# Kernel tuning notes

Measured on AMD Instinct MI355X. Metric: run time of the kernel, lower is better.

Reference implementation:

```python
import jax, jax.numpy as jnp
import numpy as np

N_NODES = 50000
N_EDGES = 800000
NFEAT = 128
NHID = 64
NLAYER = 3
BN_EPS = 1e-5


def _bn(h, gamma, beta):
    # BatchNorm1d, training-mode batch statistics (biased variance)
    mu = jnp.mean(h, axis=0)
    var = jnp.mean((h - mu) ** 2, axis=0)
    return gamma * (h - mu) * jax.lax.rsqrt(var + BN_EPS) + beta


def setup_inputs() -> dict:
    key = jax.random.key(0)
    ks = jax.random.split(key, 8)
    x = jax.random.normal(ks[0], (N_NODES, NFEAT), dtype=jnp.float32)
    edge_index = jax.random.randint(ks[1], (2, N_EDGES), 0, N_NODES, dtype=jnp.int64)
    # transform: Linear(nfeat, nhid) with bias, then BN
    W_t = jax.random.normal(ks[2], (NFEAT, NHID), dtype=jnp.float32) / np.sqrt(NFEAT)
    b_t = jnp.zeros((NHID,), dtype=jnp.float32)
    g_t = jnp.ones((NHID,), dtype=jnp.float32)
    bb_t = jnp.zeros((NHID,), dtype=jnp.float32)
    # per-layer GIN MLPs (bias=False) and BN affine params, stacked over layers
    W1 = jax.random.normal(ks[3], (NLAYER, NHID, NHID), dtype=jnp.float32) / np.sqrt(NHID)
    W2 = jax.random.normal(ks[4], (NLAYER, NHID, NHID), dtype=jnp.float32) / np.sqrt(NHID)
    gamma = jnp.ones((NLAYER, NHID), dtype=jnp.float32)
    beta = jnp.zeros((NLAYER, NHID), dtype=jnp.float32)
    return {"x": x, "edge_index": edge_index, "W_t": W_t, "b_t": b_t,
            "g_t": g_t, "bb_t": bb_t, "W1": W1, "W2": W2,
            "gamma": gamma, "beta": beta}


def reference(x, edge_index, W_t, b_t, g_t, bb_t, W1, W2, gamma, beta):
    src, dst = edge_index[0], edge_index[1]
    # input transform: Linear + BN
    h = _bn(x @ W_t + b_t, g_t, bb_t)
    for i in range(NLAYER):
        # dropout p=0 -> identity
        # GINConv (eps=0): (1+eps)*h + sum_{j->i} h_j, then 2-layer MLP
        agg = h + jax.ops.segment_sum(h[src], dst, num_segments=N_NODES)
        h = jax.nn.relu(agg @ W1[i]) @ W2[i]
        h = jax.nn.relu(h)
        h = _bn(h, gamma[i], beta[i])
    # per-graph boolean-mask split is a pure partition of rows; return full matrix
    return h
```

## Files before the change

### kernel.cpp

```cpp
#include <hip/hip_runtime.h>

#define NND 50000
#define NED 800000
#define NF  128
#define NH  64
#define BN_EPS 1e-5
#define NCOPY 8
#define SCB  256
#define NSB  ((NND + SCB - 1) / SCB)
#define XNODES (NND / 8)
#define FCH  196

#define WS_HB     0
#define WS_AGG    6400000
#define WS_STATS  12800000
#define WS_SSF    (WS_STATS + NCOPY*128*4)
#define WS_DEG    (WS_SSF + 512)
#define WS_OFFS   (WS_DEG + NND*4)
#define WS_CUR    (WS_OFFS + (NND+4)*4)
#define WS_PARTS  (WS_CUR + NND*4)
#define WS_ESRC   (WS_PARTS + 256*4)

__device__ __forceinline__ unsigned bfrn(float x) {
    unsigned u = __float_as_uint(x);
    return (u + 0x7fffu + ((u >> 16) & 1u)) >> 16;
}
__device__ __forceinline__ unsigned pk(float lo, float hi) {
    return bfrn(lo) | (bfrn(hi) << 16);
}
__device__ __forceinline__ void upadd(unsigned u, float& lo, float& hi) {
    lo += __uint_as_float(u << 16);
    hi += __uint_as_float(u & 0xffff0000u);
}
__device__ __forceinline__ float ulo(unsigned u) { return __uint_as_float(u << 16); }
__device__ __forceinline__ float uhi(unsigned u) { return __uint_as_float(u & 0xffff0000u); }

__global__ __launch_bounds__(256) void k_deg(const int* __restrict__ dst,
                                             int* __restrict__ deg) {
    int xcd = blockIdx.x & 7;
    int chunk = blockIdx.x >> 3;
    int lo = xcd * XNODES;
    const int4* d4 = (const int4*)dst;
#pragma unroll
    for (int r = 0; r < 4; ++r) {
        int i = chunk * 1024 + r * 256 + threadIdx.x;
        if (i < NED / 4) {
            int4 d = d4[i];
            if ((unsigned)(d.x - lo) < XNODES) atomicAdd(&deg[d.x], 1);
            if ((unsigned)(d.y - lo) < XNODES) atomicAdd(&deg[d.y], 1);
            if ((unsigned)(d.z - lo) < XNODES) atomicAdd(&deg[d.z], 1);
            if ((unsigned)(d.w - lo) < XNODES) atomicAdd(&deg[d.w], 1);
        }
    }
}

__global__ __launch_bounds__(256) void k_fill(const int* __restrict__ src,
                                              const int* __restrict__ dst,
                                              int* __restrict__ cur,
                                              int* __restrict__ esrc) {
    int xcd = blockIdx.x & 7;
    int chunk = blockIdx.x >> 3;
    int lo = xcd * XNODES;
    const int4* d4 = (const int4*)dst;
#pragma unroll
    for (int r = 0; r < 4; ++r) {
        int i = chunk * 1024 + r * 256 + threadIdx.x;
        if (i < NED / 4) {
            int4 d = d4[i];
            int e = i * 4;
            if ((unsigned)(d.x - lo) < XNODES) esrc[atomicAdd(&cur[d.x], 1)] = src[e];
            if ((unsigned)(d.y - lo) < XNODES) esrc[atomicAdd(&cur[d.y], 1)] = src[e + 1];
            if ((unsigned)(d.z - lo) < XNODES) esrc[atomicAdd(&cur[d.z], 1)] = src[e + 2];
            if ((unsigned)(d.w - lo) < XNODES) esrc[atomicAdd(&cur[d.w], 1)] = src[e + 3];
        }
    }
}

__global__ __launch_bounds__(SCB) void k_part(const int* __restrict__ deg,
                                              int* __restrict__ offs,
                                              int* __restrict__ parts) {
    __shared__ int sd[SCB];
    int t = threadIdx.x;
    int i = blockIdx.x * SCB + t;
    int v = (i < NND) ? deg[i] : 0;
    sd[t] = v;
    __syncthreads();
#pragma unroll
    for (int off = 1; off < SCB; off <<= 1) {
        int u = (t >= off) ? sd[t - off] : 0;
        __syncthreads();
        sd[t] += u;
        __syncthreads();
    }
    if (i < NND) offs[i] = sd[t] - v;
    if (t == SCB - 1) parts[blockIdx.x] = sd[t];
}

__global__ __launch_bounds__(256) void k_scan2(int* __restrict__ parts) {
    __shared__ int sd[256];
    int t = threadIdx.x;
    int v = (t < NSB) ? parts[t] : 0;
    sd[t] = v;
    __syncthreads();
#pragma unroll
    for (int off = 1; off < 256; off <<= 1) {
        int u = (t >= off) ? sd[t - off] : 0;
        __syncthreads();
        sd[t] += u;
        __syncthreads();
    }
    if (t < NSB) parts[t] = sd[t] - v;
}

__global__ __launch_bounds__(256) void k_apply(int* __restrict__ offs,
                                               const int* __restrict__ parts,
                                               int* __restrict__ cur) {
    int i = blockIdx.x * 256 + threadIdx.x;
    if (i < NND) {
        int o = offs[i] + parts[i >> 8];
        offs[i] = o;
        cur[i] = o;
    }
    if (i == NND) offs[NND] = NED;
}

__global__ void k_fin(float* __restrict__ st,
                      const float* __restrict__ g, const float* __restrict__ b,
                      float* __restrict__ ssout) {
    int c = threadIdx.x;
    float sum = 0.f, ssq = 0.f;
    for (int cp = 0; cp < NCOPY; ++cp) {
        sum += st[cp * 128 + c];
        ssq += st[cp * 128 + 64 + c];
    }
    for (int cp = 0; cp < NCOPY; ++cp) {
        st[cp * 128 + c] = 0.f;
        st[cp * 128 + 64 + c] = 0.f;
    }
    double mu  = (double)sum / (double)NND;
    double var = (double)ssq / (double)NND - mu * mu;
    if (var < 0.0) var = 0.0;
    double rs = 1.0 / sqrt(var + BN_EPS);
    double sc = (double)g[c] * rs;
    ssout[c]      = (float)sc;
    ssout[64 + c] = (float)((double)b[c] - mu * sc);
}

__global__ __launch_bounds__(128) void k_transform(const float* __restrict__ x,
                                                   const float* __restrict__ Wt,
                                                   const float* __restrict__ bt,
                                                   unsigned* __restrict__ hB,
                                                   float* __restrict__ stats) {
    __shared__ __align__(16) float Wl[NF * NH];
    __shared__ __align__(16) float sT[64 * 68];
    int tid  = threadIdx.x;
    int wave = tid >> 6, lane = tid & 63;
    int ti = lane & 7, tj = lane >> 3;
    int tile = blockIdx.x;
    int base = tile * 64;
    const float4* x4 = (const float4*)x;

#pragma unroll
    for (int r = 0; r < 16; ++r) {
        int i4 = r * 128 + tid;
        ((float4*)Wl)[i4] = ((const float4*)Wt)[i4];
    }

    float acc[8][4];
#pragma unroll
    for (int i = 0; i < 8; ++i)
#pragma unroll
        for (int j = 0; j < 4; ++j) acc[i][j] = 0.f;

    int cw = wave * 32 + tj * 4;

    for (int ch = 0; ch < 2; ++ch) {
        __syncthreads();
#pragma unroll
        for (int s = 0; s < 8; ++s) {
            int flat = s * 128 + tid;
            int nl = flat >> 4, q = flat & 15;
            float4 v = {0.f, 0.f, 0.f, 0.f};
            if (base + nl < NND) v = x4[(size_t)(base + nl) * 32 + ch * 16 + q];
            sT[(q * 4 + 0) * 68 + nl] = v.x;
            sT[(q * 4 + 1) * 68 + nl] = v.y;
            sT[(q * 4 + 2) * 68 + nl] = v.z;
            sT[(q * 4 + 3) * 68 + nl] = v.w;
        }
        __syncthreads();
#pragma unroll 4
        for (int k = 0; k < 64; ++k) {
            const float* ap = &sT[k * 68 + ti * 8];
            float4 alo = *(const float4*)ap;
            float4 ahi = *(const float4*)(ap + 4);
            float4 wv  = *(const float4*)&Wl[(ch * 64 + k) * NH + cw];
            float a8[8] = {alo.x, alo.y, alo.z, alo.w, ahi.x, ahi.y, ahi.z, ahi.w};
            float w4[4] = {wv.x, wv.y, wv.z, wv.w};
#pragma unroll
            for (int i = 0; i < 8; ++i)
#pragma unroll
                for (int j = 0; j < 4; ++j) acc[i][j] += a8[i] * w4[j];
        }
    }

    float4 bv = *(const float4*)&bt[cw];
    float bj[4] = {bv.x, bv.y, bv.z, bv.w};

    float s4[4] = {0.f, 0.f, 0.f, 0.f}, q4[4] = {0.f, 0.f, 0.f, 0.f};
    uint2* hB2 = (uint2*)hB;
#pragma unroll
    for (int i = 0; i < 8; ++i) {
        int n = base + ti * 8 + i;
        if (n < NND) {
            float o[4];
#pragma unroll
            for (int j = 0; j < 4; ++j) {
                o[j] = acc[i][j] + bj[j];
                s4[j] += o[j];
                q4[j] += o[j] * o[j];
            }
            uint2 ov; ov.x = pk(o[0], o[1]); ov.y = pk(o[2], o[3]);
            hB2[(size_t)n * 16 + wave * 8 + tj] = ov;
        }
    }
#pragma unroll
    for (int m = 1; m < 8; m <<= 1) {
#pragma unroll
        for (int j = 0; j < 4; ++j) {
            s4[j] += __shfl_xor(s4[j], m);
            q4[j] += __shfl_xor(q4[j], m);
        }
    }
    if (ti == 0) {
        int slot = (tile & (NCOPY - 1)) * 128;
#pragma unroll
        for (int j = 0; j < 4; ++j) {
            atomicAdd(&stats[slot + cw + j], s4[j]);
            atomicAdd(&stats[slot + 64 + cw + j], q4[j]);
        }
    }
}

__global__ __launch_bounds__(256) void k_agg(const uint4* __restrict__ hB4,
                                             uint4* __restrict__ aggB4,
                                             const float* __restrict__ ss,
                                             const int* __restrict__ offs,
                                             const int* __restrict__ esrc) {
    int tid  = threadIdx.x;
    int lane = tid & 63;
    int wv   = tid >> 6;
    int n = blockIdx.x * 4 + wv;
    int q = lane & 7;
    int r = lane >> 3;

    int e0 = offs[n], e1 = offs[n + 1];
    int deg = e1 - e0;

    float a[8];
#pragma unroll
    for (int i = 0; i < 8; ++i) a[i] = 0.f;

    if (r == 0) {
        uint4 u = hB4[(size_t)n * 8 + q];
        upadd(u.x, a[0], a[1]); upadd(u.y, a[2], a[3]);
        upadd(u.z, a[4], a[5]); upadd(u.w, a[6], a[7]);
    }

    for (int bb = e0; bb < e1; bb += 64) {
        int m = e1 - bb; if (m > 64) m = 64;
        int idx = (lane < m) ? esrc[bb + lane] : 0;
        int t = 0;
        for (; t + 32 <= m; t += 32) {
            int j0 = __shfl(idx, t + r);
            int j1 = __shfl(idx, t + 8 + r);
            int j2 = __shfl(idx, t + 16 + r);
            int j3 = __shfl(idx, t + 24 + r);
            uint4 u0 = hB4[(size_t)j0 * 8 + q];
            uint4 u1 = hB4[(size_t)j1 * 8 + q];
            uint4 u2 = hB4[(size_t)j2 * 8 + q];
            uint4 u3 = hB4[(size_t)j3 * 8 + q];
            upadd(u0.x, a[0], a[1]); upadd(u0.y, a[2], a[3]);
            upadd(u0.z, a[4], a[5]); upadd(u0.w, a[6], a[7]);
            upadd(u1.x, a[0], a[1]); upadd(u1.y, a[2], a[3]);
            upadd(u1.z, a[4], a[5]); upadd(u1.w, a[6], a[7]);
            upadd(u2.x, a[0], a[1]); upadd(u2.y, a[2], a[3]);
            upadd(u2.z, a[4], a[5]); upadd(u2.w, a[6], a[7]);
            upadd(u3.x, a[0], a[1]); upadd(u3.y, a[2], a[3]);
            upadd(u3.z, a[4], a[5]); upadd(u3.w, a[6], a[7]);
        }
        for (; t < m; t += 8) {
            int e = t + r;
            int j = __shfl(idx, e & 63);
            if (e < m) {
                uint4 u = hB4[(size_t)j * 8 + q];
                upadd(u.x, a[0], a[1]); upadd(u.y, a[2], a[3]);
                upadd(u.z, a[4], a[5]); upadd(u.w, a[6], a[7]);
            }
        }
    }

#pragma unroll
    for (int msk = 8; msk <= 32; msk <<= 1)
#pragma unroll
        for (int i = 0; i < 8; ++i) a[i] += __shfl_xor(a[i], msk);

    if (r == 0) {
        float4 scA = ((const float4*)ss)[q * 2];
        float4 scB = ((const float4*)ss)[q * 2 + 1];
        float4 shA = ((const float4*)(ss + 64))[q * 2];
        float4 shB = ((const float4*)(ss + 64))[q * 2 + 1];
        float dn = (float)(deg + 1);
        float r0 = scA.x * a[0] + dn * shA.x;
        float r1 = scA.y * a[1] + dn * shA.y;
        float r2 = scA.z * a[2] + dn * shA.z;
        float r3 = scA.w * a[3] + dn * shA.w;
        float r4 = scB.x * a[4] + dn * shB.x;
        float r5 = scB.y * a[5] + dn * shB.y;
        float r6 = scB.z * a[6] + dn * shB.z;
        float r7 = scB.w * a[7] + dn * shB.w;
        uint4 ov;
        ov.x = pk(r0, r1); ov.y = pk(r2, r3); ov.z = pk(r4, r5); ov.w = pk(r6, r7);
        aggB4[(size_t)n * 8 + q] = ov;
    }
}

__global__ __launch_bounds__(128) void k_mlp(const uint4* __restrict__ aggB4,
                                             float* __restrict__ outF,
                                             unsigned* __restrict__ hBo,
                                             float* __restrict__ stats,
                                             const float* __restrict__ W1,
                                             const float* __restrict__ W2) {
    __shared__ __align__(16) float W1l[NH * NH];
    __shared__ __align__(16) float W2l[NH * NH];
    __shared__ __align__(16) float sT[64 * 68];
    int tid  = threadIdx.x;
    int wave = tid >> 6, lane = tid & 63;
    int ti = lane & 7, tj = lane >> 3;
    int tile = blockIdx.x;
    int base = tile * 64;
    int cw = wave * 32 + tj * 4;

#pragma unroll
    for (int r = 0; r < 8; ++r) {
        int i4 = r * 128 + tid;
        ((float4*)W1l)[i4] = ((const float4*)W1)[i4];
        ((float4*)W2l)[i4] = ((const float4*)W2)[i4];
    }
#pragma unroll
    for (int s = 0; s < 4; ++s) {
        int i4 = s * 128 + tid;
        int nl = i4 >> 3, q = i4 & 7;
        uint4 u = make_uint4(0u, 0u, 0u, 0u);
        if (base + nl < NND) u = aggB4[(size_t)(base + nl) * 8 + q];
        sT[(q * 8 + 0) * 68 + nl] = ulo(u.x);
        sT[(q * 8 + 1) * 68 + nl] = uhi(u.x);
        sT[(q * 8 + 2) * 68 + nl] = ulo(u.y);
        sT[(q * 8 + 3) * 68 + nl] = uhi(u.y);
        sT[(q * 8 + 4) * 68 + nl] = ulo(u.z);
        sT[(q * 8 + 5) * 68 + nl] = uhi(u.z);
        sT[(q * 8 + 6) * 68 + nl] = ulo(u.w);
        sT[(q * 8 + 7) * 68 + nl] = uhi(u.w);
    }
    __syncthreads();

    float a1[8][4];
#pragma unroll
    for (int i = 0; i < 8; ++i)
#pragma unroll
        for (int j = 0; j < 4; ++j) a1[i][j] = 0.f;
#pragma unroll 4
    for (int k = 0; k < 64; ++k) {
        const float* ap = &sT[k * 68 + ti * 8];
        float4 alo = *(const float4*)ap;
        float4 ahi = *(const float4*)(ap + 4);
        float4 wv  = *(const float4*)&W1l[k * NH + cw];
        float a8[8] = {alo.x, alo.y, alo.z, alo.w, ahi.x, ahi.y, ahi.z, ahi.w};
        float w4[4] = {wv.x, wv.y, wv.z, wv.w};
#pragma unroll
        for (int i = 0; i < 8; ++i)
#pragma unroll
            for (int j = 0; j < 4; ++j) a1[i][j] += a8[i] * w4[j];
    }
#pragma unroll
    for (int i = 0; i < 8; ++i)
#pragma unroll
        for (int j = 0; j < 4; ++j) a1[i][j] = fmaxf(a1[i][j], 0.f);

    __syncthreads();
#pragma unroll
    for (int j = 0; j < 4; ++j) {
        float* p = &sT[(cw + j) * 68 + ti * 8];
        float4 lo = {a1[0][j], a1[1][j], a1[2][j], a1[3][j]};
        float4 hi = {a1[4][j], a1[5][j], a1[6][j], a1[7][j]};
        *(float4*)p = lo;
        *(float4*)(p + 4) = hi;
    }
    __syncthreads();

    float a2[8][4];
#pragma unroll
    for (int i = 0; i < 8; ++i)
#pragma unroll
        for (int j = 0; j < 4; ++j) a2[i][j] = 0.f;
#pragma unroll 4
    for (int k = 0; k < 64; ++k) {
        const float* ap = &sT[k * 68 + ti * 8];
        float4 alo = *(const float4*)ap;
        float4 ahi = *(const float4*)(ap + 4);
        float4 wv  = *(const float4*)&W2l[k * NH + cw];
        float a8[8] = {alo.x, alo.y, alo.z, alo.w, ahi.x, ahi.y, ahi.z, ahi.w};
        float w4[4] = {wv.x, wv.y, wv.z, wv.w};
#pragma unroll
        for (int i = 0; i < 8; ++i)
#pragma unroll
            for (int j = 0; j < 4; ++j) a2[i][j] += a8[i] * w4[j];
    }

    float s4[4] = {0.f, 0.f, 0.f, 0.f}, q4[4] = {0.f, 0.f, 0.f, 0.f};
    uint2* hBo2 = (uint2*)hBo;
#pragma unroll
    for (int i = 0; i < 8; ++i) {
        int n = base + ti * 8 + i;
        if (n < NND) {
            float o[4];
#pragma unroll
            for (int j = 0; j < 4; ++j) {
                o[j] = fmaxf(a2[i][j], 0.f);
                s4[j] += o[j];
                q4[j] += o[j] * o[j];
            }
            if (outF) *(float4*)&outF[(size_t)n * NH + cw] = *(float4*)&o[0];
            if (hBo) {
                uint2 ov; ov.x = pk(o[0], o[1]); ov.y = pk(o[2], o[3]);
                hBo2[(size_t)n * 16 + wave * 8 + tj] = ov;
            }
        }
    }
#pragma unroll
    for (int m = 1; m < 8; m <<= 1) {
#pragma unroll
        for (int j = 0; j < 4; ++j) {
            s4[j] += __shfl_xor(s4[j], m);
            q4[j] += __shfl_xor(q4[j], m);
        }
    }
    if (ti == 0) {
        int slot = (tile & (NCOPY - 1)) * 128;
#pragma unroll
        for (int j = 0; j < 4; ++j) {
            atomicAdd(&stats[slot + cw + j], s4[j]);
            atomicAdd(&stats[slot + 64 + cw + j], q4[j]);
        }
    }
}

__global__ void k_bnout(float* __restrict__ h, const float* __restrict__ ss) {
    int i4 = blockIdx.x * 256 + threadIdx.x;
    if (i4 < NND * NH / 4) {
        int cg = i4 & 15;
        float4 v   = ((float4*)h)[i4];
        float4 scv = ((const float4*)ss)[cg];
        float4 shv = ((const float4*)(ss + 64))[cg];
        v.x = v.x * scv.x + shv.x;
        v.y = v.y * scv.y + shv.y;
        v.z = v.z * scv.z + shv.z;
        v.w = v.w * scv.w + shv.w;
        ((float4*)h)[i4] = v;
    }
}

extern "C" void kernel_launch(void* const* d_in, const int* in_sizes, int n_in,
                              void* d_out, int out_size, void* d_ws, size_t ws_size,
                              hipStream_t stream) {
    const float* x     = (const float*)d_in[0];
    const int*   ei    = (const int*)d_in[1];
    const float* Wt    = (const float*)d_in[2];
    const float* bt    = (const float*)d_in[3];
    const float* gt    = (const float*)d_in[4];
    const float* bbt   = (const float*)d_in[5];
    const float* W1    = (const float*)d_in[6];
    const float* W2    = (const float*)d_in[7];
    const float* gamma = (const float*)d_in[8];
    const float* beta  = (const float*)d_in[9];
    float* out = (float*)d_out;

    char* ws = (char*)d_ws;
    unsigned* hB    = (unsigned*)(ws + WS_HB);
    unsigned* aggB  = (unsigned*)(ws + WS_AGG);
    float*    stats = (float*)(ws + WS_STATS);
    float*    ssf   = (float*)(ws + WS_SSF);
    int*      deg   = (int*)(ws + WS_DEG);
    int*      offs  = (int*)(ws + WS_OFFS);
    int*      cur   = (int*)(ws + WS_CUR);
    int*      parts = (int*)(ws + WS_PARTS);
    int*      esrc  = (int*)(ws + WS_ESRC);

    const int* srcv = ei;
    const int* dstv = ei + NED;

    hipMemsetAsync(stats, 0, NCOPY * 128 * 4 + 512 + NND * 4, stream);

    const int PGRID = FCH * 8;
    k_deg<<<PGRID, 256, 0, stream>>>(dstv, deg);
    k_part<<<NSB, SCB, 0, stream>>>(deg, offs, parts);
    k_scan2<<<1, 256, 0, stream>>>(parts);
    k_apply<<<NSB, 256, 0, stream>>>(offs, parts, cur);
    k_fill<<<PGRID, 256, 0, stream>>>(srcv, dstv, cur, esrc);

    const int NT = 782;
    const int NB = NND / 4;

    k_transform<<<NT, 128, 0, stream>>>(x, Wt, bt, hB, stats);
    k_fin<<<1, 64, 0, stream>>>(stats, gt, bbt, ssf);

    k_agg<<<NB, 256, 0, stream>>>((const uint4*)hB, (uint4*)aggB, ssf, offs, esrc);
    k_mlp<<<NT, 128, 0, stream>>>((const uint4*)aggB, nullptr, hB, stats, W1, W2);
    k_fin<<<1, 64, 0, stream>>>(stats, gamma, beta, ssf);

    k_agg<<<NB, 256, 0, stream>>>((const uint4*)hB, (uint4*)aggB, ssf, offs, esrc);
    k_mlp<<<NT, 128, 0, stream>>>((const uint4*)aggB, nullptr, hB, stats, W1 + 4096, W2 + 4096);
    k_fin<<<1, 64, 0, stream>>>(stats, gamma + 64, beta + 64, ssf);

    k_agg<<<NB, 256, 0, stream>>>((const uint4*)hB, (uint4*)aggB, ssf, offs, esrc);
    k_mlp<<<NT, 128, 0, stream>>>((const uint4*)aggB, out, nullptr, stats, W1 + 8192, W2 + 8192);
    k_fin<<<1, 64, 0, stream>>>(stats, gamma + 128, beta + 128, ssf);

    k_bnout<<<(NND * NH / 4 + 255) / 256, 256, 0, stream>>>(out, ssf);
}
```

Before: 311.6 us.

## Fold BN finalize into consumers, drop k_fin launches, use bf16 weights in transform

Removes the four single-block k_fin launches. Each k_agg wave and each k_bnout block now recomputes the BN scale and shift from per-layer stats buffers, which are kept separate so they need no zeroing between layers. The transform kernel also stores its weights as bf16 in shared memory, loads x rows into registers before the shared-memory transpose, and the edge-index loads use vectorised non-temporal reads. The cost is redundant BN derivation, including double-precision math, in every wave of the aggregation kernel, plus rounding of the transform weights to bf16.

```diff
diff --git a/kernel.cpp b/kernel.cpp
--- a/kernel.cpp
+++ b/kernel.cpp
@@ -14,13 +14,14 @@
 #define WS_HB     0
 #define WS_AGG    6400000
 #define WS_STATS  12800000
-#define WS_SSF    (WS_STATS + NCOPY*128*4)
-#define WS_DEG    (WS_SSF + 512)
+#define WS_DEG    (WS_STATS + 4*NCOPY*128*4)
 #define WS_OFFS   (WS_DEG + NND*4)
 #define WS_CUR    (WS_OFFS + (NND+4)*4)
 #define WS_PARTS  (WS_CUR + NND*4)
 #define WS_ESRC   (WS_PARTS + 256*4)
 
+typedef int int4v __attribute__((ext_vector_type(4)));
+
 __device__ __forceinline__ unsigned bfrn(float x) {
     unsigned u = __float_as_uint(x);
     return (u + 0x7fffu + ((u >> 16) & 1u)) >> 16;
@@ -34,18 +35,37 @@
 }
 __device__ __forceinline__ float ulo(unsigned u) { return __uint_as_float(u << 16); }
 __device__ __forceinline__ float uhi(unsigned u) { return __uint_as_float(u & 0xffff0000u); }
+
+__device__ __forceinline__ void bn_derive(const float* __restrict__ st, int c,
+                                          const float* __restrict__ g,
+                                          const float* __restrict__ b,
+                                          float& sc, float& sh) {
+    float sum = 0.f, ssq = 0.f;
+#pragma unroll
+    for (int cp = 0; cp < NCOPY; ++cp) {
+        sum += st[cp * 128 + c];
+        ssq += st[cp * 128 + 64 + c];
+    }
+    double mu  = (double)sum / (double)NND;
+    double var = (double)ssq / (double)NND - mu * mu;
+    if (var < 0.0) var = 0.0;
+    double rs = 1.0 / sqrt(var + BN_EPS);
+    double scd = (double)g[c] * rs;
+    sc = (float)scd;
+    sh = (float)((double)b[c] - mu * scd);
+}
 
 __global__ __launch_bounds__(256) void k_deg(const int* __restrict__ dst,
                                              int* __restrict__ deg) {
     int xcd = blockIdx.x & 7;
     int chunk = blockIdx.x >> 3;
     int lo = xcd * XNODES;
-    const int4* d4 = (const int4*)dst;
+    const int4v* d4 = (const int4v*)dst;
 #pragma unroll
     for (int r = 0; r < 4; ++r) {
         int i = chunk * 1024 + r * 256 + threadIdx.x;
         if (i < NED / 4) {
-            int4 d = d4[i];
+            int4v d = __builtin_nontemporal_load(d4 + i);
             if ((unsigned)(d.x - lo) < XNODES) atomicAdd(&deg[d.x], 1);
             if ((unsigned)(d.y - lo) < XNODES) atomicAdd(&deg[d.y], 1);
             if ((unsigned)(d.z - lo) < XNODES) atomicAdd(&deg[d.z], 1);
@@ -61,17 +81,18 @@
     int xcd = blockIdx.x & 7;
     int chunk = blockIdx.x >> 3;
     int lo = xcd * XNODES;
-    const int4* d4 = (const int4*)dst;
+    const int4v* d4 = (const int4v*)dst;
+    const int4v* s4 = (const int4v*)src;
 #pragma unroll
     for (int r = 0; r < 4; ++r) {
         int i = chunk * 1024 + r * 256 + threadIdx.x;
         if (i < NED / 4) {
-            int4 d = d4[i];
-            int e = i * 4;
-            if ((unsigned)(d.x - lo) < XNODES) esrc[atomicAdd(&cur[d.x], 1)] = src[e];
-            if ((unsigned)(d.y - lo) < XNODES) esrc[atomicAdd(&cur[d.y], 1)] = src[e + 1];
-            if ((unsigned)(d.z - lo) < XNODES) esrc[atomicAdd(&cur[d.z], 1)] = src[e + 2];
-            if ((unsigned)(d.w - lo) < XNODES) esrc[atomicAdd(&cur[d.w], 1)] = src[e + 3];
+            int4v d = __builtin_nontemporal_load(d4 + i);
+            int4v s = __builtin_nontemporal_load(s4 + i);
+            if ((unsigned)(d.x - lo) < XNODES) esrc[atomicAdd(&cur[d.x], 1)] = s.x;
+            if ((unsigned)(d.y - lo) < XNODES) esrc[atomicAdd(&cur[d.y], 1)] = s.y;
+            if ((unsigned)(d.z - lo) < XNODES) esrc[atomicAdd(&cur[d.z], 1)] = s.z;
+            if ((unsigned)(d.w - lo) < XNODES) esrc[atomicAdd(&cur[d.w], 1)] = s.w;
         }
     }
 }
@@ -124,34 +145,12 @@
     if (i == NND) offs[NND] = NED;
 }
 
-__global__ void k_fin(float* __restrict__ st,
-                      const float* __restrict__ g, const float* __restrict__ b,
-                      float* __restrict__ ssout) {
-    int c = threadIdx.x;
-    float sum = 0.f, ssq = 0.f;
-    for (int cp = 0; cp < NCOPY; ++cp) {
-        sum += st[cp * 128 + c];
-        ssq += st[cp * 128 + 64 + c];
-    }
-    for (int cp = 0; cp < NCOPY; ++cp) {
-        st[cp * 128 + c] = 0.f;
-        st[cp * 128 + 64 + c] = 0.f;
-    }
-    double mu  = (double)sum / (double)NND;
-    double var = (double)ssq / (double)NND - mu * mu;
-    if (var < 0.0) var = 0.0;
-    double rs = 1.0 / sqrt(var + BN_EPS);
-    double sc = (double)g[c] * rs;
-    ssout[c]      = (float)sc;
-    ssout[64 + c] = (float)((double)b[c] - mu * sc);
-}
-
 __global__ __launch_bounds__(128) void k_transform(const float* __restrict__ x,
                                                    const float* __restrict__ Wt,
                                                    const float* __restrict__ bt,
                                                    unsigned* __restrict__ hB,
                                                    float* __restrict__ stats) {
-    __shared__ __align__(16) float Wl[NF * NH];
+    __shared__ __align__(16) unsigned Wlu[NF * NH / 2];
     __shared__ __align__(16) float sT[64 * 68];
     int tid  = threadIdx.x;
     int wave = tid >> 6, lane = tid & 63;
@@ -163,7 +162,9 @@
 #pragma unroll
     for (int r = 0; r < 16; ++r) {
         int i4 = r * 128 + tid;
-        ((float4*)Wl)[i4] = ((const float4*)Wt)[i4];
+        float4 w = ((const float4*)Wt)[i4];
+        uint2 wp; wp.x = pk(w.x, w.y); wp.y = pk(w.z, w.w);
+        ((uint2*)Wlu)[i4] = wp;
     }
 
     float acc[8][4];
@@ -176,16 +177,22 @@
 
     for (int ch = 0; ch < 2; ++ch) {
         __syncthreads();
+        float4 pf[8];
 #pragma unroll
         for (int s = 0; s < 8; ++s) {
             int flat = s * 128 + tid;
             int nl = flat >> 4, q = flat & 15;
-            float4 v = {0.f, 0.f, 0.f, 0.f};
-            if (base + nl < NND) v = x4[(size_t)(base + nl) * 32 + ch * 16 + q];
-            sT[(q * 4 + 0) * 68 + nl] = v.x;
-            sT[(q * 4 + 1) * 68 + nl] = v.y;
-            sT[(q * 4 + 2) * 68 + nl] = v.z;
-            sT[(q * 4 + 3) * 68 + nl] = v.w;
+            pf[s] = make_float4(0.f, 0.f, 0.f, 0.f);
+            if (base + nl < NND) pf[s] = x4[(size_t)(base + nl) * 32 + ch * 16 + q];
+        }
+#pragma unroll
+        for (int s = 0; s < 8; ++s) {
+            int flat = s * 128 + tid;
+            int nl = flat >> 4, q = flat & 15;
+            sT[(q * 4 + 0) * 68 + nl] = pf[s].x;
+            sT[(q * 4 + 1) * 68 + nl] = pf[s].y;
+            sT[(q * 4 + 2) * 68 + nl] = pf[s].z;
+            sT[(q * 4 + 3) * 68 + nl] = pf[s].w;
         }
         __syncthreads();
 #pragma unroll 4
@@ -193,9 +200,9 @@
             const float* ap = &sT[k * 68 + ti * 8];
             float4 alo = *(const float4*)ap;
             float4 ahi = *(const float4*)(ap + 4);
-            float4 wv  = *(const float4*)&Wl[(ch * 64 + k) * NH + cw];
+            uint2 wu = *(const uint2*)&Wlu[(ch * 64 + k) * 32 + (cw >> 1)];
             float a8[8] = {alo.x, alo.y, alo.z, alo.w, ahi.x, ahi.y, ahi.z, ahi.w};
-            float w4[4] = {wv.x, wv.y, wv.z, wv.w};
+            float w4[4] = {ulo(wu.x), uhi(wu.x), ulo(wu.y), uhi(wu.y)};
 #pragma unroll
             for (int i = 0; i < 8; ++i)
 #pragma unroll
@@ -243,7 +250,9 @@
 
 __global__ __launch_bounds__(256) void k_agg(const uint4* __restrict__ hB4,
                                              uint4* __restrict__ aggB4,
-                                             const float* __restrict__ ss,
+                                             const float* __restrict__ stats,
+                                             const float* __restrict__ g,
+                                             const float* __restrict__ b,
                                              const int* __restrict__ offs,
                                              const int* __restrict__ esrc) {
     int tid  = threadIdx.x;
@@ -252,6 +261,9 @@
     int n = blockIdx.x * 4 + wv;
     int q = lane & 7;
     int r = lane >> 3;
+
+    float scl, shl;
+    bn_derive(stats, lane, g, b, scl, shl);
 
     int e0 = offs[n], e1 = offs[n + 1];
     int deg = e1 - e0;
@@ -304,22 +316,21 @@
 #pragma unroll
         for (int i = 0; i < 8; ++i) a[i] += __shfl_xor(a[i], msk);
 
+    float sc8[8], sh8[8];
+#pragma unroll
+    for (int j = 0; j < 8; ++j) {
+        sc8[j] = __shfl(scl, q * 8 + j);
+        sh8[j] = __shfl(shl, q * 8 + j);
+    }
+
     if (r == 0) {
-        float4 scA = ((const float4*)ss)[q * 2];
-        float4 scB = ((const float4*)ss)[q * 2 + 1];
-        float4 shA = ((const float4*)(ss + 64))[q * 2];
-        float4 shB = ((const float4*)(ss + 64))[q * 2 + 1];
         float dn = (float)(deg + 1);
-        float r0 = scA.x * a[0] + dn * shA.x;
-        float r1 = scA.y * a[1] + dn * shA.y;
-        float r2 = scA.z * a[2] + dn * shA.z;
-        float r3 = scA.w * a[3] + dn * shA.w;
-        float r4 = scB.x * a[4] + dn * shB.x;
-        float r5 = scB.y * a[5] + dn * shB.y;
-        float r6 = scB.z * a[6] + dn * shB.z;
-        float r7 = scB.w * a[7] + dn * shB.w;
+        float o[8];
+#pragma unroll
+        for (int j = 0; j < 8; ++j) o[j] = sc8[j] * a[j] + dn * sh8[j];
         uint4 ov;
-        ov.x = pk(r0, r1); ov.y = pk(r2, r3); ov.z = pk(r4, r5); ov.w = pk(r6, r7);
+        ov.x = pk(o[0], o[1]); ov.y = pk(o[2], o[3]);
+        ov.z = pk(o[4], o[5]); ov.w = pk(o[6], o[7]);
         aggB4[(size_t)n * 8 + q] = ov;
     }
 }
@@ -454,13 +465,25 @@
     }
 }
 
-__global__ void k_bnout(float* __restrict__ h, const float* __restrict__ ss) {
-    int i4 = blockIdx.x * 256 + threadIdx.x;
+__global__ __launch_bounds__(256) void k_bnout(float* __restrict__ h,
+                                               const float* __restrict__ stats,
+                                               const float* __restrict__ g,
+                                               const float* __restrict__ b) {
+    __shared__ float sl[128];
+    int tid = threadIdx.x;
+    if (tid < 64) {
+        float sc, sh;
+        bn_derive(stats, tid, g, b, sc, sh);
+        sl[tid]      = sc;
+        sl[64 + tid] = sh;
+    }
+    __syncthreads();
+    int i4 = blockIdx.x * 256 + tid;
     if (i4 < NND * NH / 4) {
         int cg = i4 & 15;
         float4 v   = ((float4*)h)[i4];
-        float4 scv = ((const float4*)ss)[cg];
-        float4 shv = ((const float4*)(ss + 64))[cg];
+        float4 scv = *(float4*)&sl[cg * 4];
+        float4 shv = *(float4*)&sl[64 + cg * 4];
         v.x = v.x * scv.x + shv.x;
         v.y = v.y * scv.y + shv.y;
         v.z = v.z * scv.z + shv.z;
@@ -488,17 +511,21 @@
     unsigned* hB    = (unsigned*)(ws + WS_HB);
     unsigned* aggB  = (unsigned*)(ws + WS_AGG);
     float*    stats = (float*)(ws + WS_STATS);
-    float*    ssf   = (float*)(ws + WS_SSF);
     int*      deg   = (int*)(ws + WS_DEG);
     int*      offs  = (int*)(ws + WS_OFFS);
     int*      cur   = (int*)(ws + WS_CUR);
     int*      parts = (int*)(ws + WS_PARTS);
     int*      esrc  = (int*)(ws + WS_ESRC);
 
+    float* st0 = stats;
+    float* st1 = stats + NCOPY * 128;
+    float* st2 = stats + 2 * NCOPY * 128;
+    float* st3 = stats + 3 * NCOPY * 128;
+
     const int* srcv = ei;
     const int* dstv = ei + NED;
 
-    hipMemsetAsync(stats, 0, NCOPY * 128 * 4 + 512 + NND * 4, stream);
+    hipMemsetAsync(stats, 0, 4 * NCOPY * 128 * 4 + NND * 4, stream);
 
     const int PGRID = FCH * 8;
     k_deg<<<PGRID, 256, 0, stream>>>(dstv, deg);
@@ -510,20 +537,16 @@
     const int NT = 782;
     const int NB = NND / 4;
 
-    k_transform<<<NT, 128, 0, stream>>>(x, Wt, bt, hB, stats);
-    k_fin<<<1, 64, 0, stream>>>(stats, gt, bbt, ssf);
-
-    k_agg<<<NB, 256, 0, stream>>>((const uint4*)hB, (uint4*)aggB, ssf, offs, esrc);
-    k_mlp<<<NT, 128, 0, stream>>>((const uint4*)aggB, nullptr, hB, stats, W1, W2);
-    k_fin<<<1, 64, 0, stream>>>(stats, gamma, beta, ssf);
-
-    k_agg<<<NB, 256, 0, stream>>>((const uint4*)hB, (uint4*)aggB, ssf, offs, esrc);
-    k_mlp<<<NT, 128, 0, stream>>>((const uint4*)aggB, nullptr, hB, stats, W1 + 4096, W2 + 4096);
-    k_fin<<<1, 64, 0, stream>>>(stats, gamma + 64, beta + 64, ssf);
-
-    k_agg<<<NB, 256, 0, stream>>>((const uint4*)hB, (uint4*)aggB, ssf, offs, esrc);
-    k_mlp<<<NT, 128, 0, stream>>>((const uint4*)aggB, out, nullptr, stats, W1 + 8192, W2 + 8192);
-    k_fin<<<1, 64, 0, stream>>>(stats, gamma + 128, beta + 128, ssf);
-
-    k_bnout<<<(NND * NH / 4 + 255) / 256, 256, 0, stream>>>(out, ssf);
-}
+    k_transform<<<NT, 128, 0, stream>>>(x, Wt, bt, hB, st0);
+
+    k_agg<<<NB, 256, 0, stream>>>((const uint4*)hB, (uint4*)aggB, st0, gt, bbt, offs, esrc);
+    k_mlp<<<NT, 128, 0, stream>>>((const uint4*)aggB, nullptr, hB, st1, W1, W2);
+
+    k_agg<<<NB, 256, 0, stream>>>((const uint4*)hB, (uint4*)aggB, st1, gamma, beta, offs, esrc);
+    k_mlp<<<NT, 128, 0, stream>>>((const uint4*)aggB, nullptr, hB, st2, W1 + 4096, W2 + 4096);
+
+    k_agg<<<NB, 256, 0, stream>>>((const uint4*)hB, (uint4*)aggB, st2, gamma + 64, beta + 64, offs, esrc);
+    k_mlp<<<NT, 128, 0, stream>>>((const uint4*)aggB, out, nullptr, st3, W1 + 8192, W2 + 8192);
+
+    k_bnout<<<(NND * NH / 4 + 255) / 256, 256, 0, stream>>>(out, st3, gamma + 128, beta + 128);
+}
```

New measurement: 323.3 us. +3.8%, slower.
